# Kernel tuning notes

Hardware: AMD Instinct MI355X
Metric: run time of the kernel (lower is better)

The kernel has to match this reference:

```python
import jax, jax.numpy as jnp
import numpy as np

B, S, C, MID = 32, 8192, 256, 128

def setup_inputs() -> dict:
    key = jax.random.key(0)
    k_x, k_w1, k_b1, k_w2, k_b2 = jax.random.split(key, 5)
    bound1 = 1.0 / np.sqrt(C)
    bound2 = 1.0 / np.sqrt(MID)
    return {
        "x": jax.random.normal(k_x, (B, S, C), dtype=jnp.float32),
        "W1": jax.random.uniform(k_w1, (C, MID), jnp.float32, -bound1, bound1),
        "b1": jax.random.uniform(k_b1, (MID,), jnp.float32, -bound1, bound1),
        "w2": jax.random.uniform(k_w2, (MID,), jnp.float32, -bound2, bound2),
        "b2": jax.random.uniform(k_b2, (), jnp.float32, -bound2, bound2),
    }

def reference(x, W1, b1, w2, b2):
    # scores: (B, S) — dropout is identity in eval mode
    h = jnp.tanh(jnp.einsum("bsc,cm->bsm", x, W1) + b1)       # (B, S, MID)
    scores = jnp.einsum("bsm,m->bs", h, w2) + b2              # (B, S)
    attn = jax.nn.softmax(scores, axis=-1)                    # softmax over seq
    out = jnp.einsum("bsc,bs->bc", x, attn)                   # weighted sum over seq
    return out
```

## Files before the change

### kernel.cpp

```cpp
#include <hip/hip_runtime.h>
#include <hip/hip_bf16.h>


typedef __attribute__((ext_vector_type(8))) short short8;
typedef __attribute__((ext_vector_type(4))) float f32x4;
typedef unsigned short u16;

constexpr int Bb = 32;
constexpr int Ss = 8192;
constexpr int Cc = 256;
constexpr int MIDm = 128;
constexpr int BM = 32;
constexpr int NBLK = Bb * Ss / BM;
constexpr int BPB = Ss / BM;

__device__ __forceinline__ u16 f2bf(float f) {
  return __builtin_bit_cast(u16, __float2bfloat16(f));
}

__global__ __launch_bounds__(256) void wprep_kernel(
    const float* __restrict__ W1, u16* __restrict__ FB)
{
  const int t    = blockIdx.x * 256 + threadIdx.x;
  const int lane = t & 63;
  const int nt   = (t >> 6) & 7;
  const int kc   = (t >> 9) & 7;
  const int n    = nt * 16 + (lane & 15);
  const int k0   = kc * 32 + (lane >> 4) * 8;
  union { u16 v[8]; short8 s; } u;
  #pragma unroll
  for (int e = 0; e < 8; ++e) u.v[e] = f2bf(W1[(size_t)(k0 + e) * MIDm + n]);
  *(short8*)(FB + (size_t)t * 8) = u.s;
}

__global__ __launch_bounds__(128, 2) void fused_kernel(
    const float* __restrict__ x, const u16* __restrict__ FB,
    const float* __restrict__ b1, const float* __restrict__ w2,
    float* __restrict__ oPart, float* __restrict__ mPart, float* __restrict__ lPart)
{
  __shared__ __align__(16) char tile[2 * 16 * 1024];
  __shared__ float sScore[BM];
  __shared__ float sP[BM];
  __shared__ float sO[2][Cc];
  __shared__ float sML[2];

  const int tid  = threadIdx.x;
  const int lane = tid & 63;
  const int w    = tid >> 6;
  const int q    = lane >> 4;
  const int ln   = lane & 15;
  const int row0 = blockIdx.x * BM;
  const int wrow0 = row0 + w * 16;

  char* ldsw = tile + w * 16384;

  {
    const char* xb = (const char*)x + (size_t)wrow0 * 1024;
    #pragma unroll
    for (int i = 0; i < 16; ++i) {
      const char* src = xb + (size_t)i * 1024 + ((lane * 16) ^ ((i & 7) << 4));
      __builtin_amdgcn_global_load_lds(
          (const __attribute__((address_space(1))) void*)src,
          (__attribute__((address_space(3))) void*)(ldsw + i * 1024),
          16, 0, 0);
    }
  }

  f32x4 acc[8];
  #pragma unroll
  for (int nt = 0; nt < 8; ++nt) {
    float bj = b1[nt * 16 + ln];
    acc[nt][0] = bj; acc[nt][1] = bj; acc[nt][2] = bj; acc[nt][3] = bj;
  }

  short8 Bf[2][8];
  #define LDB(ph, kc_)                                                        \
    { _Pragma("unroll")                                                       \
      for (int nt = 0; nt < 8; ++nt)                                          \
        Bf[ph][nt] = *(const short8*)(FB + ((size_t)((kc_) * 8 + nt) * 64 + lane) * 8); }

  LDB(0, 0)

  __builtin_amdgcn_sched_barrier(0);
  asm volatile("s_waitcnt vmcnt(0)" ::: "memory");
  __builtin_amdgcn_sched_barrier(0);

  const int sw = (ln & 7) << 4;
  const char* abase = ldsw + ln * 1024;

  #pragma unroll
  for (int kc = 0; kc < 8; ++kc) {
    const int ph = kc & 1;
    if (kc < 7) LDB(1 - ph, kc + 1)
    const int off = kc * 128 + q * 32;
    float4 lo = *(const float4*)(abase + (off ^ sw));
    float4 hi = *(const float4*)(abase + ((off + 16) ^ sw));
    union { u16 v[8]; short8 s8; } t8;
    t8.v[0] = f2bf(lo.x); t8.v[1] = f2bf(lo.y); t8.v[2] = f2bf(lo.z); t8.v[3] = f2bf(lo.w);
    t8.v[4] = f2bf(hi.x); t8.v[5] = f2bf(hi.y); t8.v[6] = f2bf(hi.z); t8.v[7] = f2bf(hi.w);
    #pragma unroll
    for (int nt = 0; nt < 8; ++nt)
      acc[nt] = __builtin_amdgcn_mfma_f32_16x16x32_bf16(t8.s8, Bf[ph][nt], acc[nt], 0, 0, 0);
  }

  float w2v[8];
  #pragma unroll
  for (int nt = 0; nt < 8; ++nt) w2v[nt] = w2[nt * 16 + ln];

  float p[4] = {0.f, 0.f, 0.f, 0.f};
  #pragma unroll
  for (int nt = 0; nt < 8; ++nt)
    #pragma unroll
    for (int r = 0; r < 4; ++r)
      p[r] += (1.0f - 2.0f / (__expf(2.0f * acc[nt][r]) + 1.0f)) * w2v[nt];

  #pragma unroll
  for (int off = 1; off < 16; off <<= 1)
    #pragma unroll
    for (int r = 0; r < 4; ++r) p[r] += __shfl_xor(p[r], off);

  if (ln == 0) {
    #pragma unroll
    for (int r = 0; r < 4; ++r) sScore[w * 16 + q * 4 + r] = p[r];
  }
  __syncthreads();

  if (w == 0) {
    float v = (lane < BM) ? sScore[lane] : -3.4e38f;
    float m = v;
    #pragma unroll
    for (int off = 1; off < 64; off <<= 1) m = fmaxf(m, __shfl_xor(m, off));
    float e = (lane < BM) ? __expf(v - m) : 0.f;
    float s = e;
    #pragma unroll
    for (int off = 1; off < 64; off <<= 1) s += __shfl_xor(s, off);
    if (lane < BM) sP[lane] = e;
    if (lane == 0) { sML[0] = m; sML[1] = s; }
  }
  __syncthreads();

  float4 o = make_float4(0.f, 0.f, 0.f, 0.f);
  #pragma unroll
  for (int i = 0; i < 16; ++i) {
    float pw = sP[w * 16 + i];
    float4 xv = *(const float4*)(ldsw + i * 1024 + ((lane * 16) ^ ((i & 7) << 4)));
    o.x = fmaf(pw, xv.x, o.x);
    o.y = fmaf(pw, xv.y, o.y);
    o.z = fmaf(pw, xv.z, o.z);
    o.w = fmaf(pw, xv.w, o.w);
  }
  *(float4*)&sO[w][lane * 4] = o;
  __syncthreads();

  {
    const int c0 = tid, c1 = tid + 128;
    float a0 = sO[0][c0] + sO[1][c0];
    float a1 = sO[0][c1] + sO[1][c1];
    float* op = oPart + (size_t)blockIdx.x * Cc;
    op[c0] = a0;
    op[c1] = a1;
  }
  if (tid == 0) { mPart[blockIdx.x] = sML[0]; lPart[blockIdx.x] = sML[1]; }
}

__global__ __launch_bounds__(256) void combine_kernel(
    const float* __restrict__ oPart, const float* __restrict__ mPart,
    const float* __restrict__ lPart, float* __restrict__ out)
{
  const int b = blockIdx.x;
  const int t = threadIdx.x;
  float M = -3.4e38f;
  for (int k = 0; k < BPB; ++k) M = fmaxf(M, mPart[b * BPB + k]);
  float num = 0.f, den = 0.f;
  for (int k = 0; k < BPB; ++k) {
    float wgt = __expf(mPart[b * BPB + k] - M);
    den += wgt * lPart[b * BPB + k];
    num = fmaf(wgt, oPart[(size_t)(b * BPB + k) * Cc + t], num);
  }
  out[b * Cc + t] = num / den;
}

extern "C" void kernel_launch(void* const* d_in, const int* in_sizes, int n_in,
                              void* d_out, int out_size, void* d_ws, size_t ws_size,
                              hipStream_t stream)
{
  const float* x  = (const float*)d_in[0];
  const float* W1 = (const float*)d_in[1];
  const float* b1 = (const float*)d_in[2];
  const float* w2 = (const float*)d_in[3];
  float* out = (float*)d_out;

  u16*   FB    = (u16*)d_ws;
  float* oPart = (float*)((char*)d_ws + 65536);
  float* mPart = (float*)((char*)d_ws + 65536 + 8388608);
  float* lPart = (float*)((char*)d_ws + 65536 + 8388608 + 32768);

  wprep_kernel<<<16, 256, 0, stream>>>(W1, FB);
  fused_kernel<<<NBLK, 128, 0, stream>>>(x, FB, b1, w2, oPart, mPart, lPart);
  combine_kernel<<<Bb, Cc, 0, stream>>>(oPart, mPart, lPart, out);
}
```

Measured before the change: 112.1 us.

## Stage W1 fragments in LDS, stream x via registers with deeper prefetch, larger row blocks

Each block now handles 128 rows with 8 waves and loads the bf16 W1 fragments into shared LDS once, instead of every wave fetching them from global memory. The x rows for the MFMA are loaded directly into registers with a 4-deep software pipeline controlled by explicit vmcnt waits, rather than waiting for a whole LDS tile. The weighted-sum pass re-reads x from global memory, relying on cache hits, and the bias add moves to the epilogue. This cuts weight traffic and the number of partials, at the cost of a second read of x and fragile hand-counted waits.

After: 95.44 us. -14.8%, faster.

```diff
diff --git a/kernel.cpp b/kernel.cpp
--- a/kernel.cpp
+++ b/kernel.cpp
@@ -10,7 +10,7 @@
 constexpr int Ss = 8192;
 constexpr int Cc = 256;
 constexpr int MIDm = 128;
-constexpr int BM = 32;
+constexpr int BM = 128;
 constexpr int NBLK = Bb * Ss / BM;
 constexpr int BPB = Ss / BM;
 
@@ -33,16 +33,12 @@
   *(short8*)(FB + (size_t)t * 8) = u.s;
 }
 
-__global__ __launch_bounds__(128, 2) void fused_kernel(
+__global__ __launch_bounds__(512, 4) void fused_kernel(
     const float* __restrict__ x, const u16* __restrict__ FB,
     const float* __restrict__ b1, const float* __restrict__ w2,
     float* __restrict__ oPart, float* __restrict__ mPart, float* __restrict__ lPart)
 {
-  __shared__ __align__(16) char tile[2 * 16 * 1024];
-  __shared__ float sScore[BM];
-  __shared__ float sP[BM];
-  __shared__ float sO[2][Cc];
-  __shared__ float sML[2];
+  __shared__ __align__(16) char smem[65536];
 
   const int tid  = threadIdx.x;
   const int lane = tid & 63;
@@ -50,70 +46,82 @@
   const int q    = lane >> 4;
   const int ln   = lane & 15;
   const int row0 = blockIdx.x * BM;
-  const int wrow0 = row0 + w * 16;
-
-  char* ldsw = tile + w * 16384;
 
   {
-    const char* xb = (const char*)x + (size_t)wrow0 * 1024;
-    #pragma unroll
-    for (int i = 0; i < 16; ++i) {
-      const char* src = xb + (size_t)i * 1024 + ((lane * 16) ^ ((i & 7) << 4));
+    const char* src = (const char*)FB + (size_t)tid * 16;
+    #pragma unroll
+    for (int i = 0; i < 8; ++i) {
       __builtin_amdgcn_global_load_lds(
-          (const __attribute__((address_space(1))) void*)src,
-          (__attribute__((address_space(3))) void*)(ldsw + i * 1024),
+          (const __attribute__((address_space(1))) void*)(src + (size_t)i * 8192),
+          (__attribute__((address_space(3))) void*)(smem + i * 8192 + tid * 16),
           16, 0, 0);
     }
   }
+  __builtin_amdgcn_sched_barrier(0);
+
+  const char* pA = (const char*)x + ((size_t)(row0 + w * 16 + ln) * Cc + q * 8) * 4;
+
+  f32x4 rA[4][2];
+  #define ISSUEA(slot, kc_)                                                         \
+    {                                                                               \
+      asm volatile("global_load_dwordx4 %0, %1, off"                                \
+                   : "=&v"(rA[slot][0]) : "v"(pA + (kc_) * 128) : "memory");        \
+      asm volatile("global_load_dwordx4 %0, %1, off"                                \
+                   : "=&v"(rA[slot][1]) : "v"(pA + (kc_) * 128 + 16) : "memory");   \
+    }
+
+  ISSUEA(0, 0) ISSUEA(1, 1) ISSUEA(2, 2) ISSUEA(3, 3)
+
+  asm volatile("s_waitcnt vmcnt(6)" ::: "memory");
+  __builtin_amdgcn_sched_barrier(0);
+  __builtin_amdgcn_s_barrier();
+  __builtin_amdgcn_sched_barrier(0);
 
   f32x4 acc[8];
   #pragma unroll
-  for (int nt = 0; nt < 8; ++nt) {
-    float bj = b1[nt * 16 + ln];
-    acc[nt][0] = bj; acc[nt][1] = bj; acc[nt][2] = bj; acc[nt][3] = bj;
-  }
-
-  short8 Bf[2][8];
-  #define LDB(ph, kc_)                                                        \
-    { _Pragma("unroll")                                                       \
-      for (int nt = 0; nt < 8; ++nt)                                          \
-        Bf[ph][nt] = *(const short8*)(FB + ((size_t)((kc_) * 8 + nt) * 64 + lane) * 8); }
-
-  LDB(0, 0)
-
-  __builtin_amdgcn_sched_barrier(0);
-  asm volatile("s_waitcnt vmcnt(0)" ::: "memory");
-  __builtin_amdgcn_sched_barrier(0);
-
-  const int sw = (ln & 7) << 4;
-  const char* abase = ldsw + ln * 1024;
+  for (int nt = 0; nt < 8; ++nt) { acc[nt][0] = 0.f; acc[nt][1] = 0.f; acc[nt][2] = 0.f; acc[nt][3] = 0.f; }
 
   #pragma unroll
   for (int kc = 0; kc < 8; ++kc) {
-    const int ph = kc & 1;
-    if (kc < 7) LDB(1 - ph, kc + 1)
-    const int off = kc * 128 + q * 32;
-    float4 lo = *(const float4*)(abase + (off ^ sw));
-    float4 hi = *(const float4*)(abase + ((off + 16) ^ sw));
+    asm volatile("s_waitcnt vmcnt(%c0)" :: "i"((kc <= 4) ? 6 : (14 - 2 * kc)) : "memory");
+    __builtin_amdgcn_sched_barrier(0);
+
+    const int slot = kc & 3;
     union { u16 v[8]; short8 s8; } t8;
-    t8.v[0] = f2bf(lo.x); t8.v[1] = f2bf(lo.y); t8.v[2] = f2bf(lo.z); t8.v[3] = f2bf(lo.w);
-    t8.v[4] = f2bf(hi.x); t8.v[5] = f2bf(hi.y); t8.v[6] = f2bf(hi.z); t8.v[7] = f2bf(hi.w);
-    #pragma unroll
-    for (int nt = 0; nt < 8; ++nt)
-      acc[nt] = __builtin_amdgcn_mfma_f32_16x16x32_bf16(t8.s8, Bf[ph][nt], acc[nt], 0, 0, 0);
-  }
-
-  float w2v[8];
-  #pragma unroll
-  for (int nt = 0; nt < 8; ++nt) w2v[nt] = w2[nt * 16 + ln];
+    t8.v[0] = f2bf(rA[slot][0][0]); t8.v[1] = f2bf(rA[slot][0][1]);
+    t8.v[2] = f2bf(rA[slot][0][2]); t8.v[3] = f2bf(rA[slot][0][3]);
+    t8.v[4] = f2bf(rA[slot][1][0]); t8.v[5] = f2bf(rA[slot][1][1]);
+    t8.v[6] = f2bf(rA[slot][1][2]); t8.v[7] = f2bf(rA[slot][1][3]);
+    const short8 af = t8.s8;
+
+    if (kc < 4) ISSUEA(slot, kc + 4)
+
+    #pragma unroll
+    for (int nt = 0; nt < 8; ++nt) {
+      short8 bf = *(const short8*)(smem + (((kc * 8 + nt) * 64 + lane) << 4));
+      acc[nt] = __builtin_amdgcn_mfma_f32_16x16x32_bf16(af, bf, acc[nt], 0, 0, 0);
+    }
+  }
+
+  __syncthreads();
+
+  float* sScore = (float*)smem;
+  float* sP     = (float*)(smem + 512);
+  float* sO     = (float*)(smem + 1024);
+  float* sML    = (float*)(smem + 9216);
+
+  float b1v[8], w2v[8];
+  #pragma unroll
+  for (int nt = 0; nt < 8; ++nt) { b1v[nt] = b1[nt * 16 + ln]; w2v[nt] = w2[nt * 16 + ln]; }
 
   float p[4] = {0.f, 0.f, 0.f, 0.f};
   #pragma unroll
   for (int nt = 0; nt < 8; ++nt)
     #pragma unroll
-    for (int r = 0; r < 4; ++r)
-      p[r] += (1.0f - 2.0f / (__expf(2.0f * acc[nt][r]) + 1.0f)) * w2v[nt];
-
+    for (int r = 0; r < 4; ++r) {
+      float h = acc[nt][r] + b1v[nt];
+      p[r] += (1.0f - 2.0f / (__expf(2.0f * h) + 1.0f)) * w2v[nt];
+    }
   #pragma unroll
   for (int off = 1; off < 16; off <<= 1)
     #pragma unroll
@@ -126,39 +134,38 @@
   __syncthreads();
 
   if (w == 0) {
-    float v = (lane < BM) ? sScore[lane] : -3.4e38f;
-    float m = v;
+    float a = sScore[lane], b = sScore[lane + 64];
+    float m = fmaxf(a, b);
     #pragma unroll
     for (int off = 1; off < 64; off <<= 1) m = fmaxf(m, __shfl_xor(m, off));
-    float e = (lane < BM) ? __expf(v - m) : 0.f;
-    float s = e;
+    float e0 = __expf(a - m), e1 = __expf(b - m);
+    sP[lane] = e0; sP[lane + 64] = e1;
+    float s = e0 + e1;
     #pragma unroll
     for (int off = 1; off < 64; off <<= 1) s += __shfl_xor(s, off);
-    if (lane < BM) sP[lane] = e;
     if (lane == 0) { sML[0] = m; sML[1] = s; }
   }
   __syncthreads();
 
+  const float* xo = x + (size_t)(row0 + w * 16) * Cc + lane * 4;
   float4 o = make_float4(0.f, 0.f, 0.f, 0.f);
-  #pragma unroll
-  for (int i = 0; i < 16; ++i) {
-    float pw = sP[w * 16 + i];
-    float4 xv = *(const float4*)(ldsw + i * 1024 + ((lane * 16) ^ ((i & 7) << 4)));
+  #pragma unroll 8
+  for (int r = 0; r < 16; ++r) {
+    float pw = sP[w * 16 + r];
+    float4 xv = *(const float4*)(xo + (size_t)r * Cc);
     o.x = fmaf(pw, xv.x, o.x);
     o.y = fmaf(pw, xv.y, o.y);
     o.z = fmaf(pw, xv.z, o.z);
     o.w = fmaf(pw, xv.w, o.w);
   }
-  *(float4*)&sO[w][lane * 4] = o;
-  __syncthreads();
-
-  {
-    const int c0 = tid, c1 = tid + 128;
-    float a0 = sO[0][c0] + sO[1][c0];
-    float a1 = sO[0][c1] + sO[1][c1];
-    float* op = oPart + (size_t)blockIdx.x * Cc;
-    op[c0] = a0;
-    op[c1] = a1;
+  *(float4*)&sO[w * Cc + lane * 4] = o;
+  __syncthreads();
+
+  if (tid < Cc) {
+    float oc = 0.f;
+    #pragma unroll
+    for (int i = 0; i < 8; ++i) oc += sO[i * Cc + tid];
+    oPart[(size_t)blockIdx.x * Cc + tid] = oc;
   }
   if (tid == 0) { mPart[blockIdx.x] = sML[0]; lPart[blockIdx.x] = sML[1]; }
 }
@@ -192,10 +199,10 @@
 
   u16*   FB    = (u16*)d_ws;
   float* oPart = (float*)((char*)d_ws + 65536);
-  float* mPart = (float*)((char*)d_ws + 65536 + 8388608);
-  float* lPart = (float*)((char*)d_ws + 65536 + 8388608 + 32768);
+  float* mPart = (float*)((char*)d_ws + 65536 + 2097152);
+  float* lPart = (float*)((char*)d_ws + 65536 + 2097152 + 8192);
 
   wprep_kernel<<<16, 256, 0, stream>>>(W1, FB);
-  fused_kernel<<<NBLK, 128, 0, stream>>>(x, FB, b1, w2, oPart, mPart, lPart);
+  fused_kernel<<<NBLK, 512, 0, stream>>>(x, FB, b1, w2, oPart, mPart, lPart);
   combine_kernel<<<Bb, Cc, 0, stream>>>(oPart, mPart, lPart, out);
 }
```

## Make fused kernel persistent with double-buffered x tiles and register-resident W1

Applied to the files above, without the earlier changes.

The fused kernel now runs 256-thread blocks that each loop over 16 tiles of 64 rows, double-buffering 64KB x tiles in LDS so the next tile's global-to-LDS load overlaps the current tile's compute. Each wave keeps its 32-column slice of the bf16 W1 fragments in registers for the whole kernel instead of reloading them per block. The MID dimension is split across the four waves, and partial scores are summed through LDS. The weighted sum over x uses shuffle reductions. This cuts weight reloads, per-block launch overhead and partial-output volume, at the cost of 128KB LDS (one block per CU), more barriers, and a shuffle-heavy reduction.

Measured after the change: 181.7 us. 62.1% more time.

```diff
diff --git a/kernel.cpp b/kernel.cpp
--- a/kernel.cpp
+++ b/kernel.cpp
@@ -10,9 +10,11 @@
 constexpr int Ss = 8192;
 constexpr int Cc = 256;
 constexpr int MIDm = 128;
-constexpr int BM = 32;
-constexpr int NBLK = Bb * Ss / BM;
-constexpr int BPB = Ss / BM;
+constexpr int TR   = 64;
+constexpr int TPB  = 16;
+constexpr int NT   = Bb * Ss / TR;
+constexpr int GRID = NT / TPB;
+constexpr int BPB  = Ss / TR;
 
 __device__ __forceinline__ u16 f2bf(float f) {
   return __builtin_bit_cast(u16, __float2bfloat16(f));
@@ -33,15 +35,15 @@
   *(short8*)(FB + (size_t)t * 8) = u.s;
 }
 
-__global__ __launch_bounds__(128, 2) void fused_kernel(
+__global__ __launch_bounds__(256, 1) void fused_kernel(
     const float* __restrict__ x, const u16* __restrict__ FB,
     const float* __restrict__ b1, const float* __restrict__ w2,
     float* __restrict__ oPart, float* __restrict__ mPart, float* __restrict__ lPart)
 {
-  __shared__ __align__(16) char tile[2 * 16 * 1024];
-  __shared__ float sScore[BM];
-  __shared__ float sP[BM];
-  __shared__ float sO[2][Cc];
+  __shared__ __align__(16) char xbuf[2 * 65536];
+  __shared__ float sSc[4][TR];
+  __shared__ float sO[4][Cc];
+  __shared__ float sP[TR];
   __shared__ float sML[2];
 
   const int tid  = threadIdx.x;
@@ -49,118 +51,141 @@
   const int w    = tid >> 6;
   const int q    = lane >> 4;
   const int ln   = lane & 15;
-  const int row0 = blockIdx.x * BM;
-  const int wrow0 = row0 + w * 16;
-
-  char* ldsw = tile + w * 16384;
-
-  {
-    const char* xb = (const char*)x + (size_t)wrow0 * 1024;
-    #pragma unroll
-    for (int i = 0; i < 16; ++i) {
-      const char* src = xb + (size_t)i * 1024 + ((lane * 16) ^ ((i & 7) << 4));
-      __builtin_amdgcn_global_load_lds(
-          (const __attribute__((address_space(1))) void*)src,
-          (__attribute__((address_space(3))) void*)(ldsw + i * 1024),
-          16, 0, 0);
-    }
+  const int gt0  = blockIdx.x * TPB;
+
+  short8 Bf[8][2];
+  #pragma unroll
+  for (int kc = 0; kc < 8; ++kc)
+    #pragma unroll
+    for (int j = 0; j < 2; ++j)
+      Bf[kc][j] = *(const short8*)(FB + ((size_t)((kc * 8 + (w * 2 + j)) * 64 + lane)) * 8);
+
+  float b1v[2], w2v[2];
+  #pragma unroll
+  for (int j = 0; j < 2; ++j) {
+    b1v[j] = b1[w * 32 + j * 16 + ln];
+    w2v[j] = w2[w * 32 + j * 16 + ln];
   }
 
-  f32x4 acc[8];
-  #pragma unroll
-  for (int nt = 0; nt < 8; ++nt) {
-    float bj = b1[nt * 16 + ln];
-    acc[nt][0] = bj; acc[nt][1] = bj; acc[nt][2] = bj; acc[nt][3] = bj;
+  #define STAGE(buf, gt)                                                              \
+    {                                                                                 \
+      _Pragma("unroll")                                                               \
+      for (int i = 0; i < 16; ++i) {                                                  \
+        const int idx  = w * 16 + i;                                                  \
+        const int kc_  = idx >> 3;                                                    \
+        const int mt_  = (idx >> 1) & 3;                                              \
+        const int hf_  = idx & 1;                                                     \
+        const char* src = (const char*)x                                              \
+            + (size_t)((gt) * TR + mt_ * 16 + ln) * 1024                              \
+            + kc_ * 128 + q * 32 + hf_ * 16;                                          \
+        __builtin_amdgcn_global_load_lds(                                             \
+            (const __attribute__((address_space(1))) void*)src,                       \
+            (__attribute__((address_space(3))) void*)                                 \
+                (xbuf + (buf) * 65536 + idx * 1024 + lane * 16),                      \
+            16, 0, 0);                                                                \
+      }                                                                               \
+    }
+
+  STAGE(0, gt0);
+
+  for (int t = 0; t < TPB; ++t) {
+    const int cur = t & 1;
+    const int gt  = gt0 + t;
+
+    if (t < TPB - 1) STAGE(cur ^ 1, gt + 1);
+
+    __builtin_amdgcn_sched_barrier(0);
+    if (t < TPB - 1) asm volatile("s_waitcnt vmcnt(16)" ::: "memory");
+    else             asm volatile("s_waitcnt vmcnt(0)"  ::: "memory");
+    __builtin_amdgcn_sched_barrier(0);
+    __builtin_amdgcn_s_barrier();
+    __builtin_amdgcn_sched_barrier(0);
+
+    const char* xb = xbuf + cur * 65536;
+
+    f32x4 acc[4][2];
+    #pragma unroll
+    for (int mt = 0; mt < 4; ++mt)
+      #pragma unroll
+      for (int j = 0; j < 2; ++j) {
+        acc[mt][j][0] = b1v[j]; acc[mt][j][1] = b1v[j];
+        acc[mt][j][2] = b1v[j]; acc[mt][j][3] = b1v[j];
+      }
+
+    #pragma unroll
+    for (int kc = 0; kc < 8; ++kc)
+      #pragma unroll
+      for (int mt = 0; mt < 4; ++mt) {
+        const char* fb = xb + kc * 8192 + mt * 2048 + lane * 16;
+        float4 lo = *(const float4*)fb;
+        float4 hi = *(const float4*)(fb + 1024);
+        union { u16 v[8]; short8 s8; } t8;
+        t8.v[0] = f2bf(lo.x); t8.v[1] = f2bf(lo.y); t8.v[2] = f2bf(lo.z); t8.v[3] = f2bf(lo.w);
+        t8.v[4] = f2bf(hi.x); t8.v[5] = f2bf(hi.y); t8.v[6] = f2bf(hi.z); t8.v[7] = f2bf(hi.w);
+        acc[mt][0] = __builtin_amdgcn_mfma_f32_16x16x32_bf16(t8.s8, Bf[kc][0], acc[mt][0], 0, 0, 0);
+        acc[mt][1] = __builtin_amdgcn_mfma_f32_16x16x32_bf16(t8.s8, Bf[kc][1], acc[mt][1], 0, 0, 0);
+      }
+
+    #pragma unroll
+    for (int mt = 0; mt < 4; ++mt) {
+      float p[4] = {0.f, 0.f, 0.f, 0.f};
+      #pragma unroll
+      for (int j = 0; j < 2; ++j)
+        #pragma unroll
+        for (int r = 0; r < 4; ++r)
+          p[r] += (1.0f - 2.0f / (__expf(2.0f * acc[mt][j][r]) + 1.0f)) * w2v[j];
+      #pragma unroll
+      for (int off = 1; off < 16; off <<= 1)
+        #pragma unroll
+        for (int r = 0; r < 4; ++r) p[r] += __shfl_xor(p[r], off);
+      if (ln == 0) {
+        #pragma unroll
+        for (int r = 0; r < 4; ++r) sSc[w][mt * 16 + q * 4 + r] = p[r];
+      }
+    }
+    __syncthreads();
+
+    if (w == 0) {
+      float v = sSc[0][lane] + sSc[1][lane] + sSc[2][lane] + sSc[3][lane];
+      float m = v;
+      #pragma unroll
+      for (int off = 1; off < 64; off <<= 1) m = fmaxf(m, __shfl_xor(m, off));
+      float e = __expf(v - m);
+      float s = e;
+      #pragma unroll
+      for (int off = 1; off < 64; off <<= 1) s += __shfl_xor(s, off);
+      sP[lane] = e;
+      if (lane == 0) { sML[0] = m; sML[1] = s; }
+    }
+    __syncthreads();
+
+    {
+      const float pw = sP[w * 16 + ln];
+      #pragma unroll
+      for (int kc = 0; kc < 8; ++kc)
+        #pragma unroll
+        for (int hf = 0; hf < 2; ++hf) {
+          const char* fb = xb + kc * 8192 + w * 2048 + hf * 1024 + lane * 16;
+          float4 v = *(const float4*)fb;
+          v.x *= pw; v.y *= pw; v.z *= pw; v.w *= pw;
+          #pragma unroll
+          for (int off = 1; off < 16; off <<= 1) {
+            v.x += __shfl_xor(v.x, off);
+            v.y += __shfl_xor(v.y, off);
+            v.z += __shfl_xor(v.z, off);
+            v.w += __shfl_xor(v.w, off);
+          }
+          if (ln == 0) *(float4*)&sO[w][kc * 32 + q * 8 + hf * 4] = v;
+        }
+    }
+    __syncthreads();
+
+    {
+      float oc = sO[0][tid & 255] + sO[1][tid & 255] + sO[2][tid & 255] + sO[3][tid & 255];
+      oPart[(size_t)gt * Cc + tid] = oc;
+    }
+    if (tid == 0) { mPart[gt] = sML[0]; lPart[gt] = sML[1]; }
   }
-
-  short8 Bf[2][8];
-  #define LDB(ph, kc_)                                                        \
-    { _Pragma("unroll")                                                       \
-      for (int nt = 0; nt < 8; ++nt)                                          \
-        Bf[ph][nt] = *(const short8*)(FB + ((size_t)((kc_) * 8 + nt) * 64 + lane) * 8); }
-
-  LDB(0, 0)
-
-  __builtin_amdgcn_sched_barrier(0);
-  asm volatile("s_waitcnt vmcnt(0)" ::: "memory");
-  __builtin_amdgcn_sched_barrier(0);
-
-  const int sw = (ln & 7) << 4;
-  const char* abase = ldsw + ln * 1024;
-
-  #pragma unroll
-  for (int kc = 0; kc < 8; ++kc) {
-    const int ph = kc & 1;
-    if (kc < 7) LDB(1 - ph, kc + 1)
-    const int off = kc * 128 + q * 32;
-    float4 lo = *(const float4*)(abase + (off ^ sw));
-    float4 hi = *(const float4*)(abase + ((off + 16) ^ sw));
-    union { u16 v[8]; short8 s8; } t8;
-    t8.v[0] = f2bf(lo.x); t8.v[1] = f2bf(lo.y); t8.v[2] = f2bf(lo.z); t8.v[3] = f2bf(lo.w);
-    t8.v[4] = f2bf(hi.x); t8.v[5] = f2bf(hi.y); t8.v[6] = f2bf(hi.z); t8.v[7] = f2bf(hi.w);
-    #pragma unroll
-    for (int nt = 0; nt < 8; ++nt)
-      acc[nt] = __builtin_amdgcn_mfma_f32_16x16x32_bf16(t8.s8, Bf[ph][nt], acc[nt], 0, 0, 0);
-  }
-
-  float w2v[8];
-  #pragma unroll
-  for (int nt = 0; nt < 8; ++nt) w2v[nt] = w2[nt * 16 + ln];
-
-  float p[4] = {0.f, 0.f, 0.f, 0.f};
-  #pragma unroll
-  for (int nt = 0; nt < 8; ++nt)
-    #pragma unroll
-    for (int r = 0; r < 4; ++r)
-      p[r] += (1.0f - 2.0f / (__expf(2.0f * acc[nt][r]) + 1.0f)) * w2v[nt];
-
-  #pragma unroll
-  for (int off = 1; off < 16; off <<= 1)
-    #pragma unroll
-    for (int r = 0; r < 4; ++r) p[r] += __shfl_xor(p[r], off);
-
-  if (ln == 0) {
-    #pragma unroll
-    for (int r = 0; r < 4; ++r) sScore[w * 16 + q * 4 + r] = p[r];
-  }
-  __syncthreads();
-
-  if (w == 0) {
-    float v = (lane < BM) ? sScore[lane] : -3.4e38f;
-    float m = v;
-    #pragma unroll
-    for (int off = 1; off < 64; off <<= 1) m = fmaxf(m, __shfl_xor(m, off));
-    float e = (lane < BM) ? __expf(v - m) : 0.f;
-    float s = e;
-    #pragma unroll
-    for (int off = 1; off < 64; off <<= 1) s += __shfl_xor(s, off);
-    if (lane < BM) sP[lane] = e;
-    if (lane == 0) { sML[0] = m; sML[1] = s; }
-  }
-  __syncthreads();
-
-  float4 o = make_float4(0.f, 0.f, 0.f, 0.f);
-  #pragma unroll
-  for (int i = 0; i < 16; ++i) {
-    float pw = sP[w * 16 + i];
-    float4 xv = *(const float4*)(ldsw + i * 1024 + ((lane * 16) ^ ((i & 7) << 4)));
-    o.x = fmaf(pw, xv.x, o.x);
-    o.y = fmaf(pw, xv.y, o.y);
-    o.z = fmaf(pw, xv.z, o.z);
-    o.w = fmaf(pw, xv.w, o.w);
-  }
-  *(float4*)&sO[w][lane * 4] = o;
-  __syncthreads();
-
-  {
-    const int c0 = tid, c1 = tid + 128;
-    float a0 = sO[0][c0] + sO[1][c0];
-    float a1 = sO[0][c1] + sO[1][c1];
-    float* op = oPart + (size_t)blockIdx.x * Cc;
-    op[c0] = a0;
-    op[c1] = a1;
-  }
-  if (tid == 0) { mPart[blockIdx.x] = sML[0]; lPart[blockIdx.x] = sML[1]; }
 }
 
 __global__ __launch_bounds__(256) void combine_kernel(
@@ -192,10 +217,10 @@
 
   u16*   FB    = (u16*)d_ws;
   float* oPart = (float*)((char*)d_ws + 65536);
-  float* mPart = (float*)((char*)d_ws + 65536 + 8388608);
-  float* lPart = (float*)((char*)d_ws + 65536 + 8388608 + 32768);
+  float* mPart = (float*)((char*)d_ws + 65536 + 4194304);
+  float* lPart = (float*)((char*)d_ws + 65536 + 4194304 + 16384);
 
   wprep_kernel<<<16, 256, 0, stream>>>(W1, FB);
-  fused_kernel<<<NBLK, 128, 0, stream>>>(x, FB, b1, w2, oPart, mPart, lPart);
+  fused_kernel<<<GRID, 256, 0, stream>>>(x, FB, b1, w2, oPart, mPart, lPart);
   combine_kernel<<<Bb, Cc, 0, stream>>>(oPart, mPart, lPart, out);
 }
```
